# Kernel tuning notes

Measured on AMD Instinct MI355X. Metric: run time of the kernel, lower is better.

The kernel has to match this reference:

```python
import jax, jax.numpy as jnp
import numpy as np

N_NODES = 20000
N_EDGES = 320000
HIDDEN = 64
HEADS = 8
HEAD_DIM = HIDDEN // HEADS
K_HOPS = 2
CST = 1e-05


def setup_inputs() -> dict:
    key = jax.random.key(0)
    ks = jax.random.split(key, 12)
    s = 1.0 / np.sqrt(HIDDEN)
    inp = {
        "x": jax.random.normal(ks[0], (N_NODES, HIDDEN), dtype=jnp.float32),
        "edge_index": jax.random.randint(ks[1], (2, N_EDGES), 0, N_NODES, dtype=jnp.int64),
        "edge_feature": jnp.zeros((1,), dtype=jnp.float32),  # unused by the module
        "Wq": jax.random.uniform(ks[2], (HIDDEN, HIDDEN), jnp.float32, -s, s),
        "bq": jax.random.uniform(ks[3], (HIDDEN,), jnp.float32, -s, s),
        "Wk": jax.random.uniform(ks[4], (HIDDEN, HIDDEN), jnp.float32, -s, s),
        "bk": jax.random.uniform(ks[5], (HIDDEN,), jnp.float32, -s, s),
        "Wv": jax.random.uniform(ks[6], (HIDDEN, HIDDEN), jnp.float32, -s, s),
        "bv": jax.random.uniform(ks[7], (HIDDEN,), jnp.float32, -s, s),
        "Wo": jax.random.uniform(ks[8], (HIDDEN, HIDDEN), jnp.float32, -s, s),
        "bo": jax.random.uniform(ks[9], (HIDDEN,), jnp.float32, -s, s),
        "hopwise": jnp.ones((K_HOPS + 1,), dtype=jnp.float32),
        "headwise": jnp.zeros((HEADS, K_HOPS), dtype=jnp.float32),
    }
    return inp


def reference(x, edge_index, edge_feature, Wq, bq, Wk, bk, Wv, bv, Wo, bo, hopwise, headwise):
    N = x.shape[0]
    row, col = edge_index[0], edge_index[1]

    # symmetric normalization: deg is in-degree of col
    deg = jax.ops.segment_sum(jnp.ones_like(col, dtype=x.dtype), col, num_segments=N)
    deg_inv = jnp.where(deg > 0, deg ** -0.5, 0.0)
    norm = deg_inv[row] * deg_inv[col]  # [E]

    Q = 1.0 + jax.nn.elu(x @ Wq + bq)
    K = 1.0 + jax.nn.elu(x @ Wk + bk)
    V = (x @ Wv + bv)
    Q = Q.reshape(N, HEADS, HEAD_DIM)
    K = K.reshape(N, HEADS, HEAD_DIM)
    V = V.reshape(N, HEADS, HEAD_DIM)

    M = jnp.einsum('nhi,nhj->nhij', K, V)  # [N,H,d,d]
    hidden = V * hopwise[0]
    layerwise = jax.nn.softmax(headwise, axis=0)  # softmax over heads (dim=-2)

    for hop in range(K_HOPS):
        # scatter-add propagation: out[i] = sum_{e: col[e]=i} norm[e] * state[row[e]]
        M = jax.ops.segment_sum(norm[:, None, None, None] * M[row], col, num_segments=N)
        K = jax.ops.segment_sum(norm[:, None, None] * K[row], col, num_segments=N)
        H = jnp.einsum('nhi,nhij->nhj', Q, M)
        C = jnp.einsum('nhi,nhi->nh', Q, K)[..., None] + CST
        H = H / C
        gamma = hopwise[hop + 1] * layerwise[:, hop][:, None]  # [H,1]
        hidden = hidden + gamma * H

    hidden = hidden.reshape(N, HEADS * HEAD_DIM)
    # dropout is identity in eval mode
    return hidden @ Wo + bo
```

## Files before the change

kernel.cpp:

```cpp
#include <hip/hip_runtime.h>
#include <hip/hip_bf16.h>

typedef __hip_bfloat16 bf16;
typedef __fp16 half2_t __attribute__((ext_vector_type(2)));
typedef float floatx2 __attribute__((ext_vector_type(2)));

#define N_NODES 20000
#define N_EDGES 320000
#define CSTF 1e-5f

#if defined(__has_builtin)
#if __has_builtin(__builtin_amdgcn_cvt_pk_fp8_f32) && __has_builtin(__builtin_amdgcn_cvt_pk_f32_fp8)
#define M1FP8 1
#endif
#if __has_builtin(__builtin_amdgcn_fdot2)
#define HAVE_FDOT2 1
#endif
#endif

#ifdef M1FP8
#define M1_STRIDE 128
#define M1_LANE   2
typedef uint2 m1vec;
#else
#define M1_STRIDE 256
#define M1_LANE   4
typedef uint4 m1vec;
#endif

__device__ __forceinline__ half2_t u2h(unsigned int u) {
    union { unsigned int u; half2_t h; } c; c.u = u; return c.h;
}
__device__ __forceinline__ unsigned int pkh(float a, float b) {
    union { __fp16 h[2]; unsigned int u; } c;
    c.h[0] = (__fp16)a; c.h[1] = (__fp16)b;
    return c.u;
}
__device__ __forceinline__ float fdot2(half2_t a, half2_t b, float c) {
#ifdef HAVE_FDOT2
    return __builtin_amdgcn_fdot2(a, b, c, false);
#else
    return fmaf((float)a.x, (float)b.x, fmaf((float)a.y, (float)b.y, c));
#endif
}
__device__ __forceinline__ int rdl(int v, int lane) { return __builtin_amdgcn_readlane(v, lane); }
__device__ __forceinline__ float ldf(const void* p, int i, bool bf) {
    return bf ? __bfloat162float(((const bf16*)p)[i]) : ((const float*)p)[i];
}
__device__ __forceinline__ bool wave_is_i64(const void* ei, int e) {
    unsigned int hi = ((const unsigned int*)ei)[2 * e + 1];
    return !__any(hi != 0);
}

struct Args {
    const void *x, *ei, *Wq, *bq, *Wk, *bk, *Wv, *bv, *Wo, *bo, *hopwise, *headwise;
    void* out;
    float* Q;
    _Float16 *K0h, *Vh, *K1h;
    unsigned int* M1h;
    int* bsrc;
    int *deg, *cnt;
};

__global__ __launch_bounds__(256) void k_p1(Args a) {
    const int t = threadIdx.x;
    const int e = blockIdx.x * 256 + t;
    bool i64 = wave_is_i64(a.ei, e);
    int r, c;
    if (i64) {
        r = (int)((const long long*)a.ei)[e];
        c = (int)((const long long*)a.ei)[N_EDGES + e];
    } else {
        r = ((const int*)a.ei)[e];
        c = ((const int*)a.ei)[N_EDGES + e];
    }
    int slot = atomicAdd(&a.deg[c], 1);
    if (slot < 64) a.bsrc[c * 64 + slot] = r;
    if (blockIdx.x < 64) {
        int bad = 0;
        for (int i = blockIdx.x * 256 + t; i < 40000; i += 64 * 256) {
            unsigned int w = ((const unsigned int*)a.x)[i];
            if (((w >> 7)  & 0xFFu) == 0xFFu) bad++;
            if (((w >> 23) & 0xFFu) == 0xFFu) bad++;
        }
        if (bad) atomicAdd(&a.cnt[0], bad);
    }
}

__global__ __launch_bounds__(256) void k_p2(Args a) {
    __shared__ __fp16 sWh[3 * 4096];
    __shared__ float sx[4][64];
    const int t = threadIdx.x;
    const bool bf = (a.cnt[0] < 16);
    for (int i = t; i < 4096; i += 256) {
        int k = i >> 6, col = i & 63;
        int di_ = (k >> 1) * 128 + col * 2 + (k & 1);
        sWh[di_]        = (__fp16)ldf(a.Wq, i, bf);
        sWh[4096 + di_] = (__fp16)ldf(a.Wk, i, bf);
        sWh[8192 + di_] = (__fp16)ldf(a.Wv, i, bf);
    }
    __syncthreads();
    const unsigned int* sWq = (const unsigned int*)sWh;
    const unsigned int* sWk = sWq + 2048;
    const unsigned int* sWv = sWq + 4096;
    const int l = t & 63, sub = t >> 6;
    const float bqv = ldf(a.bq, l, bf), bkv = ldf(a.bk, l, bf), bvv = ldf(a.bv, l, bf);
    const int n0 = blockIdx.x * 8;
    for (int g = 0; g < 2; g++) {
        int n = n0 + g * 4 + sub;
        __syncthreads();
        sx[sub][l] = ldf(a.x, n * 64 + l, bf);
        __syncthreads();
        float q = bqv, k = bkv, v = bvv;
        const float2* xp = (const float2*)sx[sub];
#pragma unroll 8
        for (int kp = 0; kp < 32; kp++) {
            float2 xv = xp[kp];
            half2_t xh = u2h(pkh(xv.x, xv.y));
            q = fdot2(xh, u2h(sWq[kp * 64 + l]), q);
            k = fdot2(xh, u2h(sWk[kp * 64 + l]), k);
            v = fdot2(xh, u2h(sWv[kp * 64 + l]), v);
        }
        int dg = a.deg[n];
        float di = dg > 0 ? rsqrtf((float)dg) : 0.0f;
        a.Q[n * 64 + l] = q > 0.0f ? q + 1.0f : __expf(q);
        float kel = k > 0.0f ? k + 1.0f : __expf(k);
        a.K0h[n * 64 + l] = (_Float16)(di * kel);
        a.Vh[n * 64 + l]  = (_Float16)v;
    }
}

__global__ __launch_bounds__(128) void k_hop1(Args a) {
    const int l = threadIdx.x & 63;
    const int n = blockIdx.x * 2 + (threadIdx.x >> 6);
    const int hb = l & 56;
    float acc[8] = {0, 0, 0, 0, 0, 0, 0, 0};
    float kacc = 0.0f;
    const int dg = a.deg[n];
    const int m = min(dg, 64);
    if (m > 0) {
        const int srcv = a.bsrc[n * 64 + (l < m ? l : m - 1)];
#define H1_BODY(KU, VO, KO)                                                \
    {                                                                      \
        half2_t p0 = u2h(KU.x), p1 = u2h(KU.y), p2 = u2h(KU.z), p3 = u2h(KU.w); \
        float vv = (float)VO;                                              \
        acc[0] = fmaf(vv, (float)p0.x, acc[0]); acc[1] = fmaf(vv, (float)p0.y, acc[1]); \
        acc[2] = fmaf(vv, (float)p1.x, acc[2]); acc[3] = fmaf(vv, (float)p1.y, acc[3]); \
        acc[4] = fmaf(vv, (float)p2.x, acc[4]); acc[5] = fmaf(vv, (float)p2.y, acc[5]); \
        acc[6] = fmaf(vv, (float)p3.x, acc[6]); acc[7] = fmaf(vv, (float)p3.y, acc[7]); \
        kacc += (float)KO;                                                 \
    }
        int e = 0;
        for (; e + 4 <= m; e += 4) {
            int sA = rdl(srcv, e), sB = rdl(srcv, e + 1), sC = rdl(srcv, e + 2), sD = rdl(srcv, e + 3);
            uint4 kA = *(const uint4*)(a.K0h + sA * 64 + hb);
            uint4 kB = *(const uint4*)(a.K0h + sB * 64 + hb);
            uint4 kC = *(const uint4*)(a.K0h + sC * 64 + hb);
            uint4 kD = *(const uint4*)(a.K0h + sD * 64 + hb);
            __fp16 vA = a.Vh[sA * 64 + l], vB = a.Vh[sB * 64 + l];
            __fp16 vC = a.Vh[sC * 64 + l], vD = a.Vh[sD * 64 + l];
            __fp16 oA = a.K0h[sA * 64 + l], oB = a.K0h[sB * 64 + l];
            __fp16 oC = a.K0h[sC * 64 + l], oD = a.K0h[sD * 64 + l];
            H1_BODY(kA, vA, oA)
            H1_BODY(kB, vB, oB)
            H1_BODY(kC, vC, oC)
            H1_BODY(kD, vD, oD)
        }
        for (; e < m; e++) {
            int sA = rdl(srcv, e);
            uint4 kA = *(const uint4*)(a.K0h + sA * 64 + hb);
            __fp16 vA = a.Vh[sA * 64 + l];
            __fp16 oA = a.K0h[sA * 64 + l];
            H1_BODY(kA, vA, oA)
        }
#undef H1_BODY
        float inv = 1.0f / (float)dg;
#pragma unroll
        for (int i = 0; i < 8; i++) acc[i] *= inv;
        kacc *= inv;
    }
#ifdef M1FP8
    unsigned int w0 = 0, w1 = 0;
    w0 = __builtin_amdgcn_cvt_pk_fp8_f32(acc[0], acc[1], w0, false);
    w0 = __builtin_amdgcn_cvt_pk_fp8_f32(acc[2], acc[3], w0, true);
    w1 = __builtin_amdgcn_cvt_pk_fp8_f32(acc[4], acc[5], w1, false);
    w1 = __builtin_amdgcn_cvt_pk_fp8_f32(acc[6], acc[7], w1, true);
    uint2 o2; o2.x = w0; o2.y = w1;
    *(uint2*)(a.M1h + (size_t)n * M1_STRIDE + l * M1_LANE) = o2;
#else
    uint4 o;
    o.x = pkh(acc[0], acc[1]); o.y = pkh(acc[2], acc[3]);
    o.z = pkh(acc[4], acc[5]); o.w = pkh(acc[6], acc[7]);
    *(uint4*)(a.M1h + (size_t)n * M1_STRIDE + l * M1_LANE) = o;
#endif
    a.K1h[n * 64 + l] = (_Float16)kacc;
}

__global__ __launch_bounds__(128) void k_hop2f(Args a) {
    const bool bf = (a.cnt[0] < 16);
    const int l = threadIdx.x & 63;
    const int n = blockIdx.x * 2 + (threadIdx.x >> 6);
    const int hb = l & 56, h = l >> 3;
    const float4 qa = *(const float4*)(a.Q + n * 64 + hb);
    const float4 qb = *(const float4*)(a.Q + n * 64 + hb + 4);
    const float qown = a.Q[n * 64 + l];
    float hacc = 0.0f, sk = 0.0f;
    const int dg = a.deg[n];
    const int m = min(dg, 64);
#ifdef M1FP8
#define H2_DOT(MU, DST)                                                    \
    {                                                                      \
        floatx2 a0 = __builtin_amdgcn_cvt_pk_f32_fp8(MU.x, false);         \
        floatx2 a1 = __builtin_amdgcn_cvt_pk_f32_fp8(MU.x, true);          \
        floatx2 a2 = __builtin_amdgcn_cvt_pk_f32_fp8(MU.y, false);         \
        floatx2 a3 = __builtin_amdgcn_cvt_pk_f32_fp8(MU.y, true);          \
        DST = qa.x * a0.x;                                                 \
        DST = fmaf(qa.y, a0.y, DST); DST = fmaf(qa.z, a1.x, DST);          \
        DST = fmaf(qa.w, a1.y, DST); DST = fmaf(qb.x, a2.x, DST);          \
        DST = fmaf(qb.y, a2.y, DST); DST = fmaf(qb.z, a3.x, DST);          \
        DST = fmaf(qb.w, a3.y, DST);                                       \
    }
#else
    const half2_t q01 = u2h(pkh(qa.x, qa.y));
    const half2_t q23 = u2h(pkh(qa.z, qa.w));
    const half2_t q45 = u2h(pkh(qb.x, qb.y));
    const half2_t q67 = u2h(pkh(qb.z, qb.w));
#define H2_DOT(MU, DST)                                                    \
    {                                                                      \
        DST = fdot2(q01, u2h(MU.x), 0.0f);                                 \
        DST = fdot2(q23, u2h(MU.y), DST);                                  \
        DST = fdot2(q45, u2h(MU.z), DST);                                  \
        DST = fdot2(q67, u2h(MU.w), DST);                                  \
    }
#endif
    if (m > 0) {
        const int srcv = a.bsrc[n * 64 + (l < m ? l : m - 1)];
        int e = 0;
        for (; e + 8 <= m; e += 8) {
            int s_[8];
            m1vec m_[8];
            __fp16 k_[8];
#pragma unroll
            for (int u = 0; u < 8; u++) s_[u] = rdl(srcv, e + u);
#pragma unroll
            for (int u = 0; u < 8; u++) m_[u] = *(const m1vec*)(a.M1h + (size_t)s_[u] * M1_STRIDE + l * M1_LANE);
#pragma unroll
            for (int u = 0; u < 8; u++) k_[u] = a.K1h[s_[u] * 64 + l];
#pragma unroll
            for (int u = 0; u < 8; u++) {
                float d;
                H2_DOT(m_[u], d)
                hacc += d;
                sk += (float)k_[u];
            }
        }
        for (; e < m; e++) {
            int sA = rdl(srcv, e);
            m1vec mA = *(const m1vec*)(a.M1h + (size_t)sA * M1_STRIDE + l * M1_LANE);
            __fp16 kA = a.K1h[sA * 64 + l];
            float d;
            H2_DOT(mA, d)
            hacc += d;
            sk += (float)kA;
        }
    }
    m1vec mo = *(const m1vec*)(a.M1h + (size_t)n * M1_STRIDE + l * M1_LANE);
    float h1r;
    H2_DOT(mo, h1r)
#undef H2_DOT
    const float din = dg > 0 ? rsqrtf((float)dg) : 0.0f;
    const float sq  = dg > 0 ? sqrtf((float)dg)  : 0.0f;
    float h1 = h1r * sq;
    float c1 = qown * (float)a.K1h[n * 64 + l];
    float c2 = qown * sk;
#pragma unroll
    for (int dd = 1; dd < 8; dd <<= 1) {
        c1 += __shfl_xor(c1, dd);
        c2 += __shfl_xor(c2, dd);
    }
    c1 *= sq;
    c2 *= din;
    float H2v = hacc * din;

    float hw0 = ldf(a.hopwise, 0, bf), hw1 = ldf(a.hopwise, 1, bf), hw2 = ldf(a.hopwise, 2, bf);
    float e0 = 0.0f, e1 = 0.0f;
#pragma unroll
    for (int hh = 0; hh < 8; hh++) {
        e0 += __expf(ldf(a.headwise, hh * 2 + 0, bf));
        e1 += __expf(ldf(a.headwise, hh * 2 + 1, bf));
    }
    float g1 = hw1 * __expf(ldf(a.headwise, h * 2 + 0, bf)) / e0;
    float g2 = hw2 * __expf(ldf(a.headwise, h * 2 + 1, bf)) / e1;

    float hidden = hw0 * (float)a.Vh[n * 64 + l] + g1 * h1 / (c1 + CSTF) + g2 * H2v / (c2 + CSTF);

    float o = ldf(a.bo, l, bf);
#pragma unroll 16
    for (int k = 0; k < 64; k++) {
        float hk = __shfl(hidden, k);
        o += hk * ldf(a.Wo, k * 64 + l, bf);
    }
    if (bf) ((bf16*)a.out)[n * 64 + l] = __float2bfloat16(o);
    else    ((float*)a.out)[n * 64 + l] = o;
}

extern "C" void kernel_launch(void* const* d_in, const int* in_sizes, int n_in,
                              void* d_out, int out_size, void* d_ws, size_t ws_size,
                              hipStream_t stream) {
    char* p = (char*)d_ws;
    auto alloc = [&](size_t bytes) {
        void* r = (void*)p;
        p += (bytes + 255) & ~(size_t)255;
        return r;
    };
    Args a;
    a.x = d_in[0];  a.ei = d_in[1];
    a.Wq = d_in[3]; a.bq = d_in[4];
    a.Wk = d_in[5]; a.bk = d_in[6];
    a.Wv = d_in[7]; a.bv = d_in[8];
    a.Wo = d_in[9]; a.bo = d_in[10];
    a.hopwise = d_in[11]; a.headwise = d_in[12];
    a.out = d_out;

    a.Q    = (float*)alloc((size_t)N_NODES * 64 * 4);
    a.K0h  = (_Float16*)alloc((size_t)N_NODES * 64 * 2);
    a.Vh   = (_Float16*)alloc((size_t)N_NODES * 64 * 2);
    a.K1h  = (_Float16*)alloc((size_t)N_NODES * 64 * 2);
    a.M1h  = (unsigned int*)alloc((size_t)N_NODES * 1024);
    a.bsrc = (int*)alloc((size_t)N_NODES * 64 * 4);
    int* zz = (int*)alloc(((size_t)N_NODES + 64) * 4);
    a.deg = zz;
    a.cnt = zz + N_NODES;

    (void)hipMemsetAsync(zz, 0, ((size_t)N_NODES + 64) * 4, stream);

    const int EB = (N_EDGES + 255) / 256;
    k_p1<<<EB, 256, 0, stream>>>(a);
    k_p2<<<2500, 256, 0, stream>>>(a);
    k_hop1<<<N_NODES / 2, 128, 0, stream>>>(a);
    k_hop2f<<<N_NODES / 2, 128, 0, stream>>>(a);
}
```

Measured before the change: 193.8 us.

## Stage Wo in fp16 LDS, precompute gamma, widen hop1 unroll, batch x loads

The final output projection now loads Wo into shared memory as packed fp16 pairs and uses fdot2 on an LDS-staged packed hidden vector, replacing 64 shuffles plus 64 global Wo loads per thread. The per-node softmax of headwise and the hopwise gammas are computed once in k_p2 block 0 and read from a small global buffer. The hop-1 gather loop is unrolled by 8 instead of 4 to keep more loads in flight. k_p2 loads all 8 x rows up front with one barrier instead of two per group. The costs are that every hop2f block of 128 threads now reloads all of Wo (4096 elements) into LDS, fp16 rounding is added to hidden and Wo, and the wider unroll raises register pressure.

```diff
diff --git a/kernel.cpp b/kernel.cpp
--- a/kernel.cpp
+++ b/kernel.cpp
@@ -59,6 +59,7 @@
     _Float16 *K0h, *Vh, *K1h;
     unsigned int* M1h;
     int* bsrc;
+    float* gbuf;
     int *deg, *cnt;
 };
 
@@ -89,9 +90,10 @@
 
 __global__ __launch_bounds__(256) void k_p2(Args a) {
     __shared__ __fp16 sWh[3 * 4096];
-    __shared__ float sx[4][64];
+    __shared__ float sx[8][64];
     const int t = threadIdx.x;
     const bool bf = (a.cnt[0] < 16);
+    const int n0 = blockIdx.x * 8;
     for (int i = t; i < 4096; i += 256) {
         int k = i >> 6, col = i & 63;
         int di_ = (k >> 1) * 128 + col * 2 + (k & 1);
@@ -99,20 +101,32 @@
         sWh[4096 + di_] = (__fp16)ldf(a.Wk, i, bf);
         sWh[8192 + di_] = (__fp16)ldf(a.Wv, i, bf);
     }
+    for (int i = t; i < 512; i += 256) {
+        int row = i >> 6, col = i & 63;
+        sx[row][col] = ldf(a.x, (n0 + row) * 64 + col, bf);
+    }
+    if (blockIdx.x == 0 && t < 8) {
+        float e0 = 0.0f, e1 = 0.0f;
+        for (int hh = 0; hh < 8; hh++) {
+            e0 += __expf(ldf(a.headwise, hh * 2 + 0, bf));
+            e1 += __expf(ldf(a.headwise, hh * 2 + 1, bf));
+        }
+        float hw1 = ldf(a.hopwise, 1, bf), hw2 = ldf(a.hopwise, 2, bf);
+        a.gbuf[t]     = hw1 * __expf(ldf(a.headwise, t * 2 + 0, bf)) / e0;
+        a.gbuf[8 + t] = hw2 * __expf(ldf(a.headwise, t * 2 + 1, bf)) / e1;
+        if (t == 0) a.gbuf[16] = ldf(a.hopwise, 0, bf);
+    }
     __syncthreads();
     const unsigned int* sWq = (const unsigned int*)sWh;
     const unsigned int* sWk = sWq + 2048;
     const unsigned int* sWv = sWq + 4096;
     const int l = t & 63, sub = t >> 6;
     const float bqv = ldf(a.bq, l, bf), bkv = ldf(a.bk, l, bf), bvv = ldf(a.bv, l, bf);
-    const int n0 = blockIdx.x * 8;
     for (int g = 0; g < 2; g++) {
-        int n = n0 + g * 4 + sub;
-        __syncthreads();
-        sx[sub][l] = ldf(a.x, n * 64 + l, bf);
-        __syncthreads();
+        int row = g * 4 + sub;
+        int n = n0 + row;
         float q = bqv, k = bkv, v = bvv;
-        const float2* xp = (const float2*)sx[sub];
+        const float2* xp = (const float2*)sx[row];
 #pragma unroll 8
         for (int kp = 0; kp < 32; kp++) {
             float2 xv = xp[kp];
@@ -140,7 +154,7 @@
     const int m = min(dg, 64);
     if (m > 0) {
         const int srcv = a.bsrc[n * 64 + (l < m ? l : m - 1)];
-#define H1_BODY(KU, VO, KO)                                                \
+#define H1_ACC(KU, VO, KO)                                                 \
     {                                                                      \
         half2_t p0 = u2h(KU.x), p1 = u2h(KU.y), p2 = u2h(KU.z), p3 = u2h(KU.w); \
         float vv = (float)VO;                                              \
@@ -151,29 +165,29 @@
         kacc += (float)KO;                                                 \
     }
         int e = 0;
-        for (; e + 4 <= m; e += 4) {
-            int sA = rdl(srcv, e), sB = rdl(srcv, e + 1), sC = rdl(srcv, e + 2), sD = rdl(srcv, e + 3);
-            uint4 kA = *(const uint4*)(a.K0h + sA * 64 + hb);
-            uint4 kB = *(const uint4*)(a.K0h + sB * 64 + hb);
-            uint4 kC = *(const uint4*)(a.K0h + sC * 64 + hb);
-            uint4 kD = *(const uint4*)(a.K0h + sD * 64 + hb);
-            __fp16 vA = a.Vh[sA * 64 + l], vB = a.Vh[sB * 64 + l];
-            __fp16 vC = a.Vh[sC * 64 + l], vD = a.Vh[sD * 64 + l];
-            __fp16 oA = a.K0h[sA * 64 + l], oB = a.K0h[sB * 64 + l];
-            __fp16 oC = a.K0h[sC * 64 + l], oD = a.K0h[sD * 64 + l];
-            H1_BODY(kA, vA, oA)
-            H1_BODY(kB, vB, oB)
-            H1_BODY(kC, vC, oC)
-            H1_BODY(kD, vD, oD)
+        for (; e + 8 <= m; e += 8) {
+            int s_[8];
+            uint4 k_[8];
+            __fp16 v_[8], o_[8];
+#pragma unroll
+            for (int u = 0; u < 8; u++) s_[u] = rdl(srcv, e + u);
+#pragma unroll
+            for (int u = 0; u < 8; u++) k_[u] = *(const uint4*)(a.K0h + s_[u] * 64 + hb);
+#pragma unroll
+            for (int u = 0; u < 8; u++) v_[u] = a.Vh[s_[u] * 64 + l];
+#pragma unroll
+            for (int u = 0; u < 8; u++) o_[u] = a.K0h[s_[u] * 64 + l];
+#pragma unroll
+            for (int u = 0; u < 8; u++) H1_ACC(k_[u], v_[u], o_[u])
         }
         for (; e < m; e++) {
             int sA = rdl(srcv, e);
             uint4 kA = *(const uint4*)(a.K0h + sA * 64 + hb);
             __fp16 vA = a.Vh[sA * 64 + l];
             __fp16 oA = a.K0h[sA * 64 + l];
-            H1_BODY(kA, vA, oA)
-        }
-#undef H1_BODY
+            H1_ACC(kA, vA, oA)
+        }
+#undef H1_ACC
         float inv = 1.0f / (float)dg;
 #pragma unroll
         for (int i = 0; i < 8; i++) acc[i] *= inv;
@@ -197,10 +211,19 @@
 }
 
 __global__ __launch_bounds__(128) void k_hop2f(Args a) {
+    __shared__ unsigned int sWo[2048];
+    __shared__ float sh[2][64];
+    __shared__ unsigned int shp[2][32];
     const bool bf = (a.cnt[0] < 16);
-    const int l = threadIdx.x & 63;
-    const int n = blockIdx.x * 2 + (threadIdx.x >> 6);
+    const int t = threadIdx.x;
+    const int l = t & 63;
+    const int w = t >> 6;
+    const int n = blockIdx.x * 2 + w;
     const int hb = l & 56, h = l >> 3;
+    for (int i = t; i < 2048; i += 128) {
+        int kp = i >> 6, c = i & 63;
+        sWo[i] = pkh(ldf(a.Wo, 2 * kp * 64 + c, bf), ldf(a.Wo, (2 * kp + 1) * 64 + c, bf));
+    }
     const float4 qa = *(const float4*)(a.Q + n * 64 + hb);
     const float4 qb = *(const float4*)(a.Q + n * 64 + hb + 4);
     const float qown = a.Q[n * 64 + l];
@@ -282,23 +305,22 @@
     c2 *= din;
     float H2v = hacc * din;
 
-    float hw0 = ldf(a.hopwise, 0, bf), hw1 = ldf(a.hopwise, 1, bf), hw2 = ldf(a.hopwise, 2, bf);
-    float e0 = 0.0f, e1 = 0.0f;
-#pragma unroll
-    for (int hh = 0; hh < 8; hh++) {
-        e0 += __expf(ldf(a.headwise, hh * 2 + 0, bf));
-        e1 += __expf(ldf(a.headwise, hh * 2 + 1, bf));
-    }
-    float g1 = hw1 * __expf(ldf(a.headwise, h * 2 + 0, bf)) / e0;
-    float g2 = hw2 * __expf(ldf(a.headwise, h * 2 + 1, bf)) / e1;
-
+    const float hw0 = a.gbuf[16];
+    const float g1 = a.gbuf[h];
+    const float g2 = a.gbuf[8 + h];
     float hidden = hw0 * (float)a.Vh[n * 64 + l] + g1 * h1 / (c1 + CSTF) + g2 * H2v / (c2 + CSTF);
 
+    sh[w][l] = hidden;
+    __syncthreads();
+    if (l < 32) {
+        float2 hp = *(const float2*)&sh[w][2 * l];
+        shp[w][l] = pkh(hp.x, hp.y);
+    }
+    __syncthreads();
     float o = ldf(a.bo, l, bf);
-#pragma unroll 16
-    for (int k = 0; k < 64; k++) {
-        float hk = __shfl(hidden, k);
-        o += hk * ldf(a.Wo, k * 64 + l, bf);
+#pragma unroll 8
+    for (int kp = 0; kp < 32; kp++) {
+        o = fdot2(u2h(shp[w][kp]), u2h(sWo[kp * 64 + l]), o);
     }
     if (bf) ((bf16*)a.out)[n * 64 + l] = __float2bfloat16(o);
     else    ((float*)a.out)[n * 64 + l] = o;
@@ -328,6 +350,7 @@
     a.K1h  = (_Float16*)alloc((size_t)N_NODES * 64 * 2);
     a.M1h  = (unsigned int*)alloc((size_t)N_NODES * 1024);
     a.bsrc = (int*)alloc((size_t)N_NODES * 64 * 4);
+    a.gbuf = (float*)alloc(32 * 4);
     int* zz = (int*)alloc(((size_t)N_NODES + 64) * 4);
     a.deg = zz;
     a.cnt = zz + N_NODES;
```

Result: slower. 201.5 us (+4.0%).
